# Optimization experiments

Hardware: AMD Instinct MI355X
Metric: run time of the kernel (lower is better)

## Reference

```python
import jax, jax.numpy as jnp
import numpy as np

NH, NKV, D = 16, 8, 128
HID = 2048
EPS = 1e-6
ROPE_BASE = 10000.0
T = 2048


def setup_inputs() -> dict:
    key = jax.random.key(0)
    k1, k2, k3 = jax.random.split(key, 3)
    return {
        "positions": jnp.arange(T, dtype=jnp.int32),
        "hidden_states": jax.random.normal(k1, (T, HID), dtype=jnp.float32),
        "w_qkv": jax.random.normal(k2, (HID, (NH + 2 * NKV) * D), dtype=jnp.float32) * 0.02,
        "w_o": jax.random.normal(k3, (NH * D, HID), dtype=jnp.float32) * 0.02,
        "q_norm_w": jnp.ones((D,), dtype=jnp.float32),
        "k_norm_w": jnp.ones((D,), dtype=jnp.float32),
    }


def _rmsnorm(x, w):
    # per-head RMSNorm over last dim (head_dim)
    return x * jax.lax.rsqrt(jnp.mean(x * x, axis=-1, keepdims=True) + EPS) * w


def reference(positions, hidden_states, w_qkv, w_o, q_norm_w, k_norm_w):
    t = hidden_states.shape[0]
    scale = D ** -0.5

    # fused QKV projection, then split
    qkv = hidden_states @ w_qkv                       # [T, (NH+2*NKV)*D]
    q, k, v = jnp.split(qkv, [NH * D, (NH + NKV) * D], axis=-1)
    q = q.reshape(t, NH, D)
    k = k.reshape(t, NKV, D)
    v = v.reshape(t, NKV, D)

    # per-head QK RMSNorm (Qwen3)
    q = _rmsnorm(q, q_norm_w)
    k = _rmsnorm(k, k_norm_w)

    # RoPE (neox style: rotate half-split pairs)
    inv_freq = 1.0 / (ROPE_BASE ** (jnp.arange(0, D, 2, dtype=jnp.float32) / D))
    freqs = positions.astype(jnp.float32)[:, None] * inv_freq  # [T, D/2]
    cos = jnp.cos(freqs)[:, None, :]                   # [T, 1, D/2]
    sin = jnp.sin(freqs)[:, None, :]

    def rope(x):
        x1, x2 = jnp.split(x, 2, axis=-1)
        return jnp.concatenate([x1 * cos - x2 * sin, x2 * cos + x1 * sin], axis=-1)

    q = rope(q)
    k = rope(k)

    # GQA: repeat kv heads
    g = NH // NKV
    kr = jnp.repeat(k, g, axis=1)                      # [T, NH, D]
    vr = jnp.repeat(v, g, axis=1)

    # causal attention
    scores = jnp.einsum('thd,shd->hts', q, kr) * scale  # [NH, T, T]
    causal = jnp.tril(jnp.ones((t, t), dtype=bool))
    scores = jnp.where(causal[None], scores, -jnp.inf)
    probs = jax.nn.softmax(scores, axis=-1)
    o = jnp.einsum('hts,shd->thd', probs, vr).reshape(t, NH * D)

    return o @ w_o
```

## Files before the change

kernel.cpp:

```cpp
#include <hip/hip_runtime.h>
#include <math.h>

#define T_TOK 2048
#define HIDDEN 2048
#define NH 16
#define NKV 8
#define DH 128

typedef unsigned short u16;
typedef __attribute__((ext_vector_type(8))) short bf16x8;
typedef __attribute__((ext_vector_type(4))) float f32x4;

__device__ __forceinline__ u16 f2bf(float f) {
  union { float f; unsigned u; } x; x.f = f;
  unsigned r = (x.u + 0x7fffu + ((x.u >> 16) & 1u)) >> 16;
  return (u16)r;
}

__device__ __forceinline__ float bf2f(u16 v) {
  union { unsigned u; float f; } x; x.u = ((unsigned)v) << 16;
  return x.f;
}

__device__ __forceinline__ void gload16(const void* g, void* l) {
  __builtin_amdgcn_global_load_lds((const __attribute__((address_space(1))) void*)g,
                                   (__attribute__((address_space(3))) void*)l,
                                   16, 0, 0);
}

__global__ __launch_bounds__(256) void prepass(const float* __restrict__ hidden,
                                               const float* __restrict__ w_qkv,
                                               const float* __restrict__ w_o,
                                               u16* __restrict__ Xb,
                                               u16* __restrict__ WqkvT,
                                               u16* __restrict__ WoT) {
  __shared__ float tile[64][65];
  const int b = blockIdx.x;
  if (b < 4096) {
    int i = b * 256 + threadIdx.x;
    float4 v = ((const float4*)hidden)[i];
    ushort4 o;
    o.x = f2bf(v.x); o.y = f2bf(v.y); o.z = f2bf(v.z); o.w = f2bf(v.w);
    ((ushort4*)Xb)[i] = o;
    return;
  }
  const float* in; u16* out; int R, Cdim, c0, r0;
  if (b < 6144) {
    int bb = b - 4096;
    in = w_qkv; out = WqkvT; R = 2048; Cdim = 4096;
    c0 = (bb & 63) * 64; r0 = (bb >> 6) * 64;
  } else {
    int bb = b - 6144;
    in = w_o; out = WoT; R = 2048; Cdim = 2048;
    c0 = (bb & 31) * 64; r0 = (bb >> 5) * 64;
  }
  const int tx = threadIdx.x & 63, ty = threadIdx.x >> 6;
#pragma unroll
  for (int i = 0; i < 64; i += 4)
    tile[ty + i][tx] = in[(size_t)(r0 + ty + i) * Cdim + c0 + tx];
  __syncthreads();
#pragma unroll
  for (int i = 0; i < 64; i += 4)
    out[(size_t)(c0 + ty + i) * R + r0 + tx] = f2bf(tile[tx][ty + i]);
}

__global__ __launch_bounds__(256) void add_parts2(const u16* __restrict__ a,
                                                  const u16* __restrict__ b,
                                                  float* __restrict__ o, int n4) {
  int i = blockIdx.x * blockDim.x + threadIdx.x;
  if (i < n4) {
    ushort4 x = ((const ushort4*)a)[i], y = ((const ushort4*)b)[i];
    float4 z;
    z.x = bf2f(x.x) + bf2f(y.x);
    z.y = bf2f(x.y) + bf2f(y.y);
    z.z = bf2f(x.z) + bf2f(y.z);
    z.w = bf2f(x.w) + bf2f(y.w);
    ((float4*)o)[i] = z;
  }
}

__global__ __launch_bounds__(256) void rope_vt(const u16* __restrict__ qkv,
                                               const int* __restrict__ pos,
                                               const float* __restrict__ qw,
                                               const float* __restrict__ kw,
                                               u16* __restrict__ Qg,
                                               u16* __restrict__ Kg,
                                               u16* __restrict__ Vt) {
  __shared__ float tile[64][65];
  const int b = blockIdx.x;
  if (b < 12288) {
    const int wave = threadIdx.x >> 6, j = threadIdx.x & 63;
    const int idx = b * 4 + wave;
    const int t = idx & 2047, slot = idx >> 11;
    const float QSC = 0.088388347648318447f * 1.4426950408889634f;
    const size_t base_i = (size_t)t * 4096 + slot * 128;
    float x1 = bf2f(qkv[base_i + j]);
    float x2 = bf2f(qkv[base_i + j + 64]);
    float ss = x1 * x1 + x2 * x2;
#pragma unroll
    for (int m = 1; m < 64; m <<= 1) ss += __shfl_xor(ss, m);
    float r = rsqrtf(ss * (1.0f / 128.0f) + 1e-6f);
    const bool isq = slot < NH;
    const float* w = isq ? qw : kw;
    float xn1 = x1 * r * w[j], xn2 = x2 * r * w[j + 64];
    float fp = (float)pos[t];
    float inv_freq = exp2f(-(float)j * (13.287712379549449f / 64.0f));
    float ang = fp * inv_freq;
    float sn, cs;
    sincosf(ang, &sn, &cs);
    float o1 = xn1 * cs - xn2 * sn;
    float o2 = xn2 * cs + xn1 * sn;
    if (isq) {
      size_t base = ((size_t)slot * T_TOK + t) * DH;
      Qg[base + j] = f2bf(o1 * QSC); Qg[base + 64 + j] = f2bf(o2 * QSC);
    } else {
      size_t base = ((size_t)(slot - NH) * T_TOK + t) * DH;
      Kg[base + j] = f2bf(o1); Kg[base + 64 + j] = f2bf(o2);
    }
    return;
  }
  const int bb = b - 12288;
  const int h = bb & 7, rest = bb >> 3;
  const int t0 = (rest & 31) * 64, d0 = (rest >> 5) * 64;
  const int tx = threadIdx.x & 63, ty = threadIdx.x >> 6;
#pragma unroll
  for (int i = 0; i < 64; i += 4) {
    size_t gi = (size_t)(t0 + ty + i) * 4096 + (NH + NKV) * DH + h * DH + d0 + tx;
    tile[ty + i][tx] = bf2f(qkv[gi]);
  }
  __syncthreads();
  const int sx = ((tx >> 5) * 2 + ((tx >> 2) & 1)) * 16 + ((tx >> 3) & 3) * 4 + (tx & 3);
#pragma unroll
  for (int i = 0; i < 64; i += 4)
    Vt[((size_t)h * DH + d0 + ty + i) * T_TOK + t0 + tx] = f2bf(tile[sx][ty + i]);
}

__global__ __launch_bounds__(512, 2) void gemm128x256(const u16* __restrict__ A,
                                                      const u16* __restrict__ Bt,
                                                      void* __restrict__ Cout,
                                                      int M, int N, int K,
                                                      int lda, int ldb, int obf16) {
  __shared__ __attribute__((aligned(128))) char lds[98304];

  const int nx = N >> 8, ny = M >> 7;
  const int flat = blockIdx.x;
  const int per = gridDim.x >> 3;
  const int swz = (flat & 7) * per + (flat >> 3);
  const int by = swz % ny;
  const int rest = swz / ny;
  const int bx = rest % nx;
  const int bz = rest / nx;
  const int m0 = by << 7, n0 = bx << 8;
  A += (size_t)bz * K;
  Bt += (size_t)bz * K;

  const int tid = threadIdx.x;
  const int wave = tid >> 6, lane = tid & 63;
  const int l15 = lane & 15, quad = lane >> 4;
  const int wr = wave >> 2, wc = wave & 3;

  size_t aoff;
  {
    int chunk = tid;
    int line = chunk >> 3;
    int ls8 = (chunk & 7) ^ (line & 7);
    int row = line * 2 + (ls8 >> 2);
    int ks = ls8 & 3;
    aoff = (size_t)(m0 + row) * lda + ks * 8;
  }
  size_t boff[2];
#pragma unroll
  for (int c = 0; c < 2; ++c) {
    int chunk = c * 512 + tid;
    int line = chunk >> 3;
    int ls8 = (chunk & 7) ^ (line & 7);
    int row = line * 2 + (ls8 >> 2);
    int ks = ls8 & 3;
    boff[c] = (size_t)(n0 + row) * ldb + ks * 8;
  }

#define STAGE(tt) do {                                                   \
    char* da = lds + ((tt) & 3) * 8192 + wave * 1024;                    \
    char* db = lds + 32768 + ((tt) & 3) * 16384 + wave * 1024;           \
    const int kk = (tt) * 32;                                            \
    gload16(A + aoff + kk, da);                                          \
    gload16(Bt + boff[0] + kk, db);                                      \
    gload16(Bt + boff[1] + kk, db + 8192);                               \
  } while (0)

  const int fragoff = (l15 >> 1) * 128 +
                      (((((l15 & 1) << 2) | quad) ^ ((l15 >> 1) & 7)) << 4);

  const f32x4 zero = {0.f, 0.f, 0.f, 0.f};
  f32x4 acc[4][4];
#pragma unroll
  for (int i = 0; i < 4; ++i)
#pragma unroll
    for (int j = 0; j < 4; ++j) acc[i][j] = zero;

  const int NT = K >> 5;
  STAGE(0); STAGE(1); STAGE(2);
  asm volatile("s_waitcnt vmcnt(6)" ::: "memory");
  __builtin_amdgcn_s_barrier();

  for (int t = 0; t < NT; ++t) {
    const char* As = lds + (t & 3) * 8192 + wr * 4096 + fragoff;
    const char* Bs = lds + 32768 + (t & 3) * 16384 + wc * 4096 + fragoff;
    bf16x8 af[4], bfr[4];
#pragma unroll
    for (int mt = 0; mt < 4; ++mt) af[mt] = *(const bf16x8*)(As + mt * 1024);
#pragma unroll
    for (int nt = 0; nt < 4; ++nt) bfr[nt] = *(const bf16x8*)(Bs + nt * 1024);

    if (t + 3 < NT) STAGE(t + 3);

    __builtin_amdgcn_s_setprio(1);
#pragma unroll
    for (int mt = 0; mt < 4; ++mt)
#pragma unroll
      for (int nt = 0; nt < 4; ++nt)
        acc[mt][nt] = __builtin_amdgcn_mfma_f32_16x16x32_bf16(af[mt], bfr[nt], acc[mt][nt], 0, 0, 0);
    __builtin_amdgcn_s_setprio(0);

    const int rem = NT - 1 - t;
    if (rem >= 3)      asm volatile("s_waitcnt vmcnt(6)" ::: "memory");
    else if (rem == 2) asm volatile("s_waitcnt vmcnt(3)" ::: "memory");
    else if (rem == 1) asm volatile("s_waitcnt vmcnt(0)" ::: "memory");
    if (rem > 0) __builtin_amdgcn_s_barrier();
  }
#undef STAGE

  if (obf16) {
    u16* C = (u16*)Cout + (size_t)bz * M * N;
#pragma unroll
    for (int mt = 0; mt < 4; ++mt)
#pragma unroll
      for (int nt = 0; nt < 4; ++nt)
#pragma unroll
        for (int r = 0; r < 4; ++r)
          C[(size_t)(m0 + wr * 64 + mt * 16 + quad * 4 + r) * N + n0 + wc * 64 + nt * 16 + l15] =
              f2bf(acc[mt][nt][r]);
  } else {
    float* C = (float*)Cout + (size_t)bz * M * N;
#pragma unroll
    for (int mt = 0; mt < 4; ++mt)
#pragma unroll
      for (int nt = 0; nt < 4; ++nt)
#pragma unroll
        for (int r = 0; r < 4; ++r)
          C[(size_t)(m0 + wr * 64 + mt * 16 + quad * 4 + r) * N + n0 + wc * 64 + nt * 16 + l15] =
              acc[mt][nt][r];
  }
}

__global__ __launch_bounds__(512) void attn_kernel(const u16* __restrict__ Qg,
                                                   const u16* __restrict__ Kg,
                                                   const u16* __restrict__ Vtg,
                                                   u16* __restrict__ Og) {
  __shared__ u16 Klds[2][64 * 128];
  __shared__ u16 Vlds[2][128 * 64];
  const int tid = threadIdx.x;
  const int wave = tid >> 6, lane = tid & 63;
  const int l15 = lane & 15, quad = lane >> 4;
  const int b = blockIdx.x;
  const int h = b & 15, pr = b >> 4;
  const int kvh = h >> 1;
  const int qtLO = pr, qtHI = 31 - pr;
  const int myqt = (wave < 4) ? qtHI : qtLO;
  const int w4 = wave & 3;
  const int jmax = qtHI + 1;
  const f32x4 zero = {0.f, 0.f, 0.f, 0.f};

  const u16* Qh = Qg + (size_t)h * T_TOK * DH;
  const u16* Kh = Kg + (size_t)kvh * T_TOK * DH;
  const u16* Vh = Vtg + (size_t)kvh * DH * T_TOK;
  const int qrow0 = myqt * 64 + w4 * 16;

#define STAGEKV(jj, sl) do {                                            \
    u16* Kd = &Klds[sl][0]; u16* Vd = &Vlds[sl][0];                     \
    _Pragma("unroll")                                                   \
    for (int c = 0; c < 2; ++c) {                                       \
      int chunk = wave * 2 + c;                                         \
      int sL = chunk * 64 + lane;                                       \
      { int ss = sL >> 4;                                               \
        int g = (sL & 15) ^ (ss & 15);                                  \
        gload16(Kh + ((size_t)((jj) * 64 + ss)) * DH + g * 8, Kd + chunk * 512); } \
      { int d = sL >> 3;                                                \
        int g = (sL & 7) ^ (d & 7);                                     \
        gload16(Vh + (size_t)d * T_TOK + (jj) * 64 + g * 8, Vd + chunk * 512); } \
    } } while (0)

  bf16x8 qf[4];
#pragma unroll
  for (int ks = 0; ks < 4; ++ks)
    qf[ks] = *(const bf16x8*)(Qh + (size_t)(qrow0 + l15) * DH + ks * 32 + quad * 8);

  f32x4 oacc[8];
#pragma unroll
  for (int i = 0; i < 8; ++i) oacc[i] = zero;
  float l_acc = 0.f;

  STAGEKV(0, 0);
  asm volatile("s_waitcnt vmcnt(0)" ::: "memory");
  __builtin_amdgcn_s_barrier();

  for (int j = 0; j < jmax; ++j) {
    const int sl = j & 1;
    const bool more = (j + 1 < jmax);
    if (more) STAGEKV(j + 1, sl ^ 1);
    if (j <= myqt) {
      const u16* Kl = &Klds[sl][0];
      const u16* Vl = &Vlds[sl][0];

      f32x4 sacc[4];
#pragma unroll
      for (int nt = 0; nt < 4; ++nt) sacc[nt] = zero;
      __builtin_amdgcn_s_setprio(1);
#pragma unroll
      for (int nt = 0; nt < 4; ++nt) {
        int sr = nt * 16 + l15;
#pragma unroll
        for (int ks = 0; ks < 4; ++ks) {
          bf16x8 kf = *(const bf16x8*)&Kl[sr * 128 + (((ks * 4 + quad) ^ (sr & 15)) * 8)];
          sacc[nt] = __builtin_amdgcn_mfma_f32_16x16x32_bf16(kf, qf[ks], sacc[nt], 0, 0, 0);
        }
      }
      __builtin_amdgcn_s_setprio(0);

      if (j >= myqt) {
        int q = qrow0 + l15;
#pragma unroll
        for (int nt = 0; nt < 4; ++nt)
#pragma unroll
          for (int r = 0; r < 4; ++r) {
            int k = j * 64 + nt * 16 + quad * 4 + r;
            if (k > q) sacc[nt][r] = -INFINITY;
          }
      }

      union { unsigned d[4]; bf16x8 v; } pa[2];
#pragma unroll
      for (int ks = 0; ks < 2; ++ks)
#pragma unroll
        for (int w = 0; w < 4; ++w) {
          int nt = ks * 2 + (w >> 1), rp = (w & 1) * 2;
          unsigned ulo = __float_as_uint(exp2f(sacc[nt][rp]));
          unsigned uhi = __float_as_uint(exp2f(sacc[nt][rp + 1]));
          l_acc += __uint_as_float(ulo & 0xffff0000u) + __uint_as_float(uhi & 0xffff0000u);
          pa[ks].d[w] = (ulo >> 16) | (uhi & 0xffff0000u);
        }

      __builtin_amdgcn_s_setprio(1);
#pragma unroll
      for (int ot = 0; ot < 8; ++ot) {
        int d = ot * 16 + l15;
#pragma unroll
        for (int ks = 0; ks < 2; ++ks) {
          bf16x8 vf = *(const bf16x8*)&Vl[d * 64 + (((ks * 4 + quad) ^ (d & 7)) * 8)];
          oacc[ot] = __builtin_amdgcn_mfma_f32_16x16x32_bf16(pa[ks].v, vf, oacc[ot], 0, 0, 0);
        }
      }
      __builtin_amdgcn_s_setprio(0);
    }

    if (more) {
      asm volatile("s_waitcnt vmcnt(0)" ::: "memory");
      __builtin_amdgcn_s_barrier();
    }
  }

  l_acc += __shfl_xor(l_acc, 16);
  l_acc += __shfl_xor(l_acc, 32);
  float rl[4];
#pragma unroll
  for (int r = 0; r < 4; ++r)
    rl[r] = 1.0f / __shfl(l_acc, quad * 4 + r);
#pragma unroll
  for (int ot = 0; ot < 8; ++ot)
#pragma unroll
    for (int r = 0; r < 4; ++r)
      Og[(size_t)(qrow0 + quad * 4 + r) * (NH * DH) + h * DH + ot * 16 + l15] =
          f2bf(oacc[ot][r] * rl[r]);
#undef STAGEKV
}

extern "C" void kernel_launch(void* const* d_in, const int* in_sizes, int n_in,
                              void* d_out, int out_size, void* d_ws, size_t ws_size,
                              hipStream_t stream) {
  (void)in_sizes; (void)n_in; (void)out_size; (void)ws_size;
  const int* positions = (const int*)d_in[0];
  const float* hidden  = (const float*)d_in[1];
  const float* w_qkv   = (const float*)d_in[2];
  const float* w_o     = (const float*)d_in[3];
  const float* q_norm  = (const float*)d_in[4];
  const float* k_norm  = (const float*)d_in[5];
  float* out = (float*)d_out;

  char* ws = (char*)d_ws;
  u16*   Xb    = (u16*)(ws);
  u16*   WqkvT = (u16*)(ws + ( 8ull << 20));
  u16*   WoT   = (u16*)(ws + (24ull << 20));
  u16*   P0    = (u16*)(ws + (32ull << 20));
  u16*   Qg    = (u16*)(ws + ( 8ull << 20));
  u16*   Kg    = (u16*)(ws + (16ull << 20));
  u16*   Vt    = (u16*)(ws + (20ull << 20));
  u16*   AttnO = (u16*)(ws + (48ull << 20));
  u16*   G2P   = (u16*)(ws + (32ull << 20));

  prepass<<<dim3(7168), 256, 0, stream>>>(hidden, w_qkv, w_o, Xb, WqkvT, WoT);

  gemm128x256<<<dim3(256), 512, 0, stream>>>(
      Xb, WqkvT, P0, T_TOK, 4096, HIDDEN, HIDDEN, HIDDEN, 1);

  rope_vt<<<dim3(12288 + 512), 256, 0, stream>>>(P0, positions,
                                                 q_norm, k_norm, Qg, Kg, Vt);

  attn_kernel<<<dim3(256), 512, 0, stream>>>(Qg, Kg, Vt, AttnO);

  gemm128x256<<<dim3(256), 512, 0, stream>>>(
      AttnO, WoT, G2P, T_TOK, HIDDEN, 1024, NH * DH, NH * DH, 1);
  const int n4 = T_TOK * HIDDEN / 4;
  add_parts2<<<dim3(n4 / 256), 256, 0, stream>>>(
      G2P, G2P + (size_t)T_TOK * HIDDEN, out, n4);
}
```

Measured before the change: 235.8 us.

## Split KV tiles across wave groups and process two query fragments per wave

The attention kernel now stages two KV tiles per iteration. The two four-wave groups each take alternate tiles, and every wave handles 32 query rows, so each K/V fragment read from LDS feeds two MFMAs. Partial outputs and row sums from the second group are combined with the first through LDS at the end. This is meant to halve the serial KV loop length per block and cut LDS reads per MFMA. The cost is double the LDS footprint, a cross-group reduction, and roughly double the accumulator registers. Under launch_bounds(512,2) that register growth could cause spills.

```diff
diff --git a/kernel.cpp b/kernel.cpp
--- a/kernel.cpp
+++ b/kernel.cpp
@@ -253,68 +253,77 @@
   }
 }
 
-__global__ __launch_bounds__(512) void attn_kernel(const u16* __restrict__ Qg,
-                                                   const u16* __restrict__ Kg,
-                                                   const u16* __restrict__ Vtg,
-                                                   u16* __restrict__ Og) {
-  __shared__ u16 Klds[2][64 * 128];
-  __shared__ u16 Vlds[2][128 * 64];
+__global__ __launch_bounds__(512, 2) void attn_kernel(const u16* __restrict__ Qg,
+                                                      const u16* __restrict__ Kg,
+                                                      const u16* __restrict__ Vtg,
+                                                      u16* __restrict__ Og) {
+  __shared__ u16 Klds[2][2][64 * 128];
+  __shared__ u16 Vlds[2][2][128 * 64];
+  __shared__ float Lx[128];
   const int tid = threadIdx.x;
   const int wave = tid >> 6, lane = tid & 63;
   const int l15 = lane & 15, quad = lane >> 4;
+  const int gp = wave >> 2, w4 = wave & 3;
   const int b = blockIdx.x;
   const int h = b & 15, pr = b >> 4;
   const int kvh = h >> 1;
-  const int qtLO = pr, qtHI = 31 - pr;
-  const int myqt = (wave < 4) ? qtHI : qtLO;
-  const int w4 = wave & 3;
+  const int qtHI = 31 - pr, qtLO = pr;
+  const int myqt = (w4 < 2) ? qtHI : qtLO;
+  const int qbase = myqt * 64 + (w4 & 1) * 32;
   const int jmax = qtHI + 1;
+  const int T = (jmax + 1) >> 1;
   const f32x4 zero = {0.f, 0.f, 0.f, 0.f};
 
   const u16* Qh = Qg + (size_t)h * T_TOK * DH;
   const u16* Kh = Kg + (size_t)kvh * T_TOK * DH;
   const u16* Vh = Vtg + (size_t)kvh * DH * T_TOK;
-  const int qrow0 = myqt * 64 + w4 * 16;
-
-#define STAGEKV(jj, sl) do {                                            \
-    u16* Kd = &Klds[sl][0]; u16* Vd = &Vlds[sl][0];                     \
+
+#define STAGEPAIR(t2, sl) do {                                          \
     _Pragma("unroll")                                                   \
-    for (int c = 0; c < 2; ++c) {                                       \
-      int chunk = wave * 2 + c;                                         \
-      int sL = chunk * 64 + lane;                                       \
+    for (int c = 0; c < 4; ++c) {                                       \
+      int cg = wave * 4 + c;                                \
+      int tp = cg >> 4;                                \
+      int cw = cg & 15;                                                 \
+      int sL = cw * 64 + lane;              \
+      int jj = (t2) + tp;                                               \
       { int ss = sL >> 4;                                               \
         int g = (sL & 15) ^ (ss & 15);                                  \
-        gload16(Kh + ((size_t)((jj) * 64 + ss)) * DH + g * 8, Kd + chunk * 512); } \
+        gload16(Kh + ((size_t)(jj * 64 + ss)) * DH + g * 8,             \
+                &Klds[sl][tp][0] + cw * 512); }                         \
       { int d = sL >> 3;                                                \
-        int g = (sL & 7) ^ (d & 7);                                     \
-        gload16(Vh + (size_t)d * T_TOK + (jj) * 64 + g * 8, Vd + chunk * 512); } \
+        int gv = (sL & 7) ^ (d & 7);                                    \
+        gload16(Vh + (size_t)d * T_TOK + jj * 64 + gv * 8,              \
+                &Vlds[sl][tp][0] + cw * 512); }                         \
     } } while (0)
 
-  bf16x8 qf[4];
-#pragma unroll
-  for (int ks = 0; ks < 4; ++ks)
-    qf[ks] = *(const bf16x8*)(Qh + (size_t)(qrow0 + l15) * DH + ks * 32 + quad * 8);
-
-  f32x4 oacc[8];
-#pragma unroll
-  for (int i = 0; i < 8; ++i) oacc[i] = zero;
-  float l_acc = 0.f;
-
-  STAGEKV(0, 0);
+  bf16x8 qfa[4], qfb[4];
+#pragma unroll
+  for (int ks = 0; ks < 4; ++ks) {
+    qfa[ks] = *(const bf16x8*)(Qh + (size_t)(qbase + l15) * DH + ks * 32 + quad * 8);
+    qfb[ks] = *(const bf16x8*)(Qh + (size_t)(qbase + 16 + l15) * DH + ks * 32 + quad * 8);
+  }
+
+  f32x4 oa[8], ob[8];
+#pragma unroll
+  for (int i = 0; i < 8; ++i) { oa[i] = zero; ob[i] = zero; }
+  float la = 0.f, lb = 0.f;
+
+  STAGEPAIR(0, 0);
   asm volatile("s_waitcnt vmcnt(0)" ::: "memory");
   __builtin_amdgcn_s_barrier();
 
-  for (int j = 0; j < jmax; ++j) {
-    const int sl = j & 1;
-    const bool more = (j + 1 < jmax);
-    if (more) STAGEKV(j + 1, sl ^ 1);
+  for (int t = 0; t < T; ++t) {
+    const int sl = t & 1;
+    const bool more = (t + 1 < T);
+    if (more) STAGEPAIR(2 * t + 2, sl ^ 1);
+    const int j = 2 * t + gp;
     if (j <= myqt) {
-      const u16* Kl = &Klds[sl][0];
-      const u16* Vl = &Vlds[sl][0];
-
-      f32x4 sacc[4];
-#pragma unroll
-      for (int nt = 0; nt < 4; ++nt) sacc[nt] = zero;
+      const u16* Kl = &Klds[sl][gp][0];
+      const u16* Vl = &Vlds[sl][gp][0];
+
+      f32x4 sa[4], sb[4];
+#pragma unroll
+      for (int nt = 0; nt < 4; ++nt) { sa[nt] = zero; sb[nt] = zero; }
       __builtin_amdgcn_s_setprio(1);
 #pragma unroll
       for (int nt = 0; nt < 4; ++nt) {
@@ -322,32 +331,38 @@
 #pragma unroll
         for (int ks = 0; ks < 4; ++ks) {
           bf16x8 kf = *(const bf16x8*)&Kl[sr * 128 + (((ks * 4 + quad) ^ (sr & 15)) * 8)];
-          sacc[nt] = __builtin_amdgcn_mfma_f32_16x16x32_bf16(kf, qf[ks], sacc[nt], 0, 0, 0);
+          sa[nt] = __builtin_amdgcn_mfma_f32_16x16x32_bf16(kf, qfa[ks], sa[nt], 0, 0, 0);
+          sb[nt] = __builtin_amdgcn_mfma_f32_16x16x32_bf16(kf, qfb[ks], sb[nt], 0, 0, 0);
         }
       }
       __builtin_amdgcn_s_setprio(0);
 
-      if (j >= myqt) {
-        int q = qrow0 + l15;
+      if (j == myqt) {
+        int qA = qbase + l15, qB = qA + 16;
 #pragma unroll
         for (int nt = 0; nt < 4; ++nt)
 #pragma unroll
           for (int r = 0; r < 4; ++r) {
             int k = j * 64 + nt * 16 + quad * 4 + r;
-            if (k > q) sacc[nt][r] = -INFINITY;
+            if (k > qA) sa[nt][r] = -INFINITY;
+            if (k > qB) sb[nt][r] = -INFINITY;
           }
       }
 
-      union { unsigned d[4]; bf16x8 v; } pa[2];
+      union { unsigned d[4]; bf16x8 v; } paA[2], paB[2];
 #pragma unroll
       for (int ks = 0; ks < 2; ++ks)
 #pragma unroll
         for (int w = 0; w < 4; ++w) {
           int nt = ks * 2 + (w >> 1), rp = (w & 1) * 2;
-          unsigned ulo = __float_as_uint(exp2f(sacc[nt][rp]));
-          unsigned uhi = __float_as_uint(exp2f(sacc[nt][rp + 1]));
-          l_acc += __uint_as_float(ulo & 0xffff0000u) + __uint_as_float(uhi & 0xffff0000u);
-          pa[ks].d[w] = (ulo >> 16) | (uhi & 0xffff0000u);
+          unsigned ulo = __float_as_uint(exp2f(sa[nt][rp]));
+          unsigned uhi = __float_as_uint(exp2f(sa[nt][rp + 1]));
+          la += __uint_as_float(ulo & 0xffff0000u) + __uint_as_float(uhi & 0xffff0000u);
+          paA[ks].d[w] = (ulo >> 16) | (uhi & 0xffff0000u);
+          unsigned vlo = __float_as_uint(exp2f(sb[nt][rp]));
+          unsigned vhi = __float_as_uint(exp2f(sb[nt][rp + 1]));
+          lb += __uint_as_float(vlo & 0xffff0000u) + __uint_as_float(vhi & 0xffff0000u);
+          paB[ks].d[w] = (vlo >> 16) | (vhi & 0xffff0000u);
         }
 
       __builtin_amdgcn_s_setprio(1);
@@ -357,7 +372,8 @@
 #pragma unroll
         for (int ks = 0; ks < 2; ++ks) {
           bf16x8 vf = *(const bf16x8*)&Vl[d * 64 + (((ks * 4 + quad) ^ (d & 7)) * 8)];
-          oacc[ot] = __builtin_amdgcn_mfma_f32_16x16x32_bf16(pa[ks].v, vf, oacc[ot], 0, 0, 0);
+          oa[ot] = __builtin_amdgcn_mfma_f32_16x16x32_bf16(paA[ks].v, vf, oa[ot], 0, 0, 0);
+          ob[ot] = __builtin_amdgcn_mfma_f32_16x16x32_bf16(paB[ks].v, vf, ob[ot], 0, 0, 0);
         }
       }
       __builtin_amdgcn_s_setprio(0);
@@ -369,19 +385,48 @@
     }
   }
 
-  l_acc += __shfl_xor(l_acc, 16);
-  l_acc += __shfl_xor(l_acc, 32);
-  float rl[4];
-#pragma unroll
-  for (int r = 0; r < 4; ++r)
-    rl[r] = 1.0f / __shfl(l_acc, quad * 4 + r);
-#pragma unroll
-  for (int ot = 0; ot < 8; ++ot)
-#pragma unroll
-    for (int r = 0; r < 4; ++r)
-      Og[(size_t)(qrow0 + quad * 4 + r) * (NH * DH) + h * DH + ot * 16 + l15] =
-          f2bf(oacc[ot][r] * rl[r]);
-#undef STAGEKV
+  la += __shfl_xor(la, 16); la += __shfl_xor(la, 32);
+  lb += __shfl_xor(lb, 16); lb += __shfl_xor(lb, 32);
+
+  __syncthreads();
+  float* Olds = (float*)&Klds[0][0][0];
+  if (gp == 1) {
+    float* Ow = Olds + (size_t)w4 * (32 * 128);
+#pragma unroll
+    for (int ot = 0; ot < 8; ++ot)
+#pragma unroll
+      for (int r = 0; r < 4; ++r) {
+        Ow[(quad * 4 + r) * 128 + ot * 16 + l15] = oa[ot][r];
+        Ow[(16 + quad * 4 + r) * 128 + ot * 16 + l15] = ob[ot][r];
+      }
+    if (quad == 0) {
+      Lx[w4 * 32 + l15] = la;
+      Lx[w4 * 32 + 16 + l15] = lb;
+    }
+  }
+  __syncthreads();
+  if (gp == 0) {
+    const float* Or = Olds + (size_t)w4 * (32 * 128);
+    float rlA[4], rlB[4];
+#pragma unroll
+    for (int r = 0; r < 4; ++r) {
+      int i = quad * 4 + r;
+      rlA[r] = 1.0f / (__shfl(la, i) + Lx[w4 * 32 + i]);
+      rlB[r] = 1.0f / (__shfl(lb, i) + Lx[w4 * 32 + 16 + i]);
+    }
+#pragma unroll
+    for (int ot = 0; ot < 8; ++ot)
+#pragma unroll
+      for (int r = 0; r < 4; ++r) {
+        int rowA = qbase + quad * 4 + r;
+        Og[(size_t)rowA * (NH * DH) + h * DH + ot * 16 + l15] =
+            f2bf((oa[ot][r] + Or[(quad * 4 + r) * 128 + ot * 16 + l15]) * rlA[r]);
+        int rowB = rowA + 16;
+        Og[(size_t)rowB * (NH * DH) + h * DH + ot * 16 + l15] =
+            f2bf((ob[ot][r] + Or[(16 + quad * 4 + r) * 128 + ot * 16 + l15]) * rlB[r]);
+      }
+  }
+#undef STAGEPAIR
 }
 
 extern "C" void kernel_launch(void* const* d_in, const int* in_sizes, int n_in,
```

After: 237.6 us. Within noise of the previous version (+0.7%).

## Rebalance causal attention work across wave groups with split-KV and LDS reduction

Applied to the files above, without the earlier changes.

In the original kernel, one wave group handles the high query tile (up to 32 KV tiles) while the other handles the low tile (few KV tiles), so half the waves sit idle for most iterations. Now both groups first process the low tile's KV tiles together. After that, the two groups split the remaining high-tile KV tiles, each taking alternate tiles from double-staged buffers, which shortens the loop to 17 steps. Partial outputs and row sums for the high tile are combined through LDS at the end. The cost is twice the LDS footprint, a second set of accumulators that raises register pressure, and an extra reduction step.

```diff
diff --git a/kernel.cpp b/kernel.cpp
--- a/kernel.cpp
+++ b/kernel.cpp
@@ -253,135 +253,193 @@
   }
 }
 
-__global__ __launch_bounds__(512) void attn_kernel(const u16* __restrict__ Qg,
-                                                   const u16* __restrict__ Kg,
-                                                   const u16* __restrict__ Vtg,
-                                                   u16* __restrict__ Og) {
-  __shared__ u16 Klds[2][64 * 128];
-  __shared__ u16 Vlds[2][128 * 64];
+__global__ __launch_bounds__(512, 2) void attn_kernel(const u16* __restrict__ Qg,
+                                                      const u16* __restrict__ Kg,
+                                                      const u16* __restrict__ Vtg,
+                                                      u16* __restrict__ Og) {
+  __shared__ u16 Klds[2][2][64 * 128];
+  __shared__ u16 Vlds[2][2][128 * 64];
+  __shared__ float Lx[64];
   const int tid = threadIdx.x;
   const int wave = tid >> 6, lane = tid & 63;
   const int l15 = lane & 15, quad = lane >> 4;
+  const int gp = wave >> 2, w4 = wave & 3;
   const int b = blockIdx.x;
   const int h = b & 15, pr = b >> 4;
   const int kvh = h >> 1;
-  const int qtLO = pr, qtHI = 31 - pr;
-  const int myqt = (wave < 4) ? qtHI : qtLO;
-  const int w4 = wave & 3;
-  const int jmax = qtHI + 1;
+  const int qtHI = 31 - pr, qtLO = pr;
   const f32x4 zero = {0.f, 0.f, 0.f, 0.f};
 
   const u16* Qh = Qg + (size_t)h * T_TOK * DH;
   const u16* Kh = Kg + (size_t)kvh * T_TOK * DH;
   const u16* Vh = Vtg + (size_t)kvh * DH * T_TOK;
-  const int qrow0 = myqt * 64 + w4 * 16;
-
-#define STAGEKV(jj, sl) do {                                            \
-    u16* Kd = &Klds[sl][0]; u16* Vd = &Vlds[sl][0];                     \
+  const int qbH = qtHI * 64 + w4 * 16;
+  const int qbL = qtLO * 64 + w4 * 16;
+
+#define STAGE1(jj, sl, ss) do {                                         \
+    u16* Kd = &Klds[sl][ss][0]; u16* Vd = &Vlds[sl][ss][0];             \
     _Pragma("unroll")                                                   \
     for (int c = 0; c < 2; ++c) {                                       \
       int chunk = wave * 2 + c;                                         \
       int sL = chunk * 64 + lane;                                       \
-      { int ss = sL >> 4;                                               \
-        int g = (sL & 15) ^ (ss & 15);                                  \
-        gload16(Kh + ((size_t)((jj) * 64 + ss)) * DH + g * 8, Kd + chunk * 512); } \
+      { int ssk = sL >> 4;                                              \
+        int g = (sL & 15) ^ (ssk & 15);                                 \
+        gload16(Kh + ((size_t)((jj) * 64 + ssk)) * DH + g * 8, Kd + chunk * 512); } \
       { int d = sL >> 3;                                                \
-        int g = (sL & 7) ^ (d & 7);                                     \
-        gload16(Vh + (size_t)d * T_TOK + (jj) * 64 + g * 8, Vd + chunk * 512); } \
+        int gv = (sL & 7) ^ (d & 7);                                    \
+        gload16(Vh + (size_t)d * T_TOK + (jj) * 64 + gv * 8, Vd + chunk * 512); } \
     } } while (0)
 
-  bf16x8 qf[4];
-#pragma unroll
-  for (int ks = 0; ks < 4; ++ks)
-    qf[ks] = *(const bf16x8*)(Qh + (size_t)(qrow0 + l15) * DH + ks * 32 + quad * 8);
-
-  f32x4 oacc[8];
-#pragma unroll
-  for (int i = 0; i < 8; ++i) oacc[i] = zero;
-  float l_acc = 0.f;
-
-  STAGEKV(0, 0);
+#define STAGESTEP(ts, sl) do {                                          \
+    if ((ts) <= pr) { STAGE1((ts), (sl), 0); }                          \
+    else {                                                              \
+      int uu = (ts) - pr - 1;                                           \
+      int jA = pr + 1 + 2 * uu;                                         \
+      STAGE1(jA, (sl), 0);                                              \
+      if (jA + 1 <= qtHI) STAGE1(jA + 1, (sl), 1);                      \
+    } } while (0)
+
+#define TILE_BODY(QF, OACC, LACC, QT, JJ, KL, VL) do {                  \
+    f32x4 sacc[4];                                                      \
+    _Pragma("unroll")                                                   \
+    for (int nt = 0; nt < 4; ++nt) sacc[nt] = zero;                     \
+    __builtin_amdgcn_s_setprio(1);                                      \
+    _Pragma("unroll")                                                   \
+    for (int nt = 0; nt < 4; ++nt) {                                    \
+      int sr = nt * 16 + l15;                                           \
+      _Pragma("unroll")                                                 \
+      for (int ks = 0; ks < 4; ++ks) {                                  \
+        bf16x8 kf = *(const bf16x8*)&(KL)[sr * 128 + (((ks * 4 + quad) ^ (sr & 15)) * 8)]; \
+        sacc[nt] = __builtin_amdgcn_mfma_f32_16x16x32_bf16(kf, (QF)[ks], sacc[nt], 0, 0, 0); \
+      }                                                                 \
+    }                                                                   \
+    __builtin_amdgcn_s_setprio(0);                                      \
+    if ((JJ) == (QT)) {                                                 \
+      int q = (QT) * 64 + w4 * 16 + l15;                                \
+      _Pragma("unroll")                                                 \
+      for (int nt = 0; nt < 4; ++nt)                                    \
+        _Pragma("unroll")                                               \
+        for (int r = 0; r < 4; ++r) {                                   \
+          int k = (JJ) * 64 + nt * 16 + quad * 4 + r;                   \
+          if (k > q) sacc[nt][r] = -INFINITY;                           \
+        }                                                               \
+    }                                                                   \
+    union { unsigned d[4]; bf16x8 v; } pa[2];                           \
+    _Pragma("unroll")                                                   \
+    for (int ks = 0; ks < 2; ++ks)                                      \
+      _Pragma("unroll")                                                 \
+      for (int w = 0; w < 4; ++w) {                                     \
+        int nt = ks * 2 + (w >> 1), rp = (w & 1) * 2;                   \
+        unsigned ulo = __float_as_uint(exp2f(sacc[nt][rp]));            \
+        unsigned uhi = __float_as_uint(exp2f(sacc[nt][rp + 1]));        \
+        (LACC) += __uint_as_float(ulo & 0xffff0000u) + __uint_as_float(uhi & 0xffff0000u); \
+        pa[ks].d[w] = (ulo >> 16) | (uhi & 0xffff0000u);                \
+      }                                                                 \
+    __builtin_amdgcn_s_setprio(1);                                      \
+    _Pragma("unroll")                                                   \
+    for (int ot = 0; ot < 8; ++ot) {                                    \
+      int d = ot * 16 + l15;                                            \
+      _Pragma("unroll")                                                 \
+      for (int ks = 0; ks < 2; ++ks) {                                  \
+        bf16x8 vf = *(const bf16x8*)&(VL)[d * 64 + (((ks * 4 + quad) ^ (d & 7)) * 8)]; \
+        (OACC)[ot] = __builtin_amdgcn_mfma_f32_16x16x32_bf16(pa[ks].v, vf, (OACC)[ot], 0, 0, 0); \
+      }                                                                 \
+    }                                                                   \
+    __builtin_amdgcn_s_setprio(0);                                      \
+  } while (0)
+
+  bf16x8 qfH[4], qfL[4];
+#pragma unroll
+  for (int ks = 0; ks < 4; ++ks) {
+    qfH[ks] = *(const bf16x8*)(Qh + (size_t)(qbH + l15) * DH + ks * 32 + quad * 8);
+    qfL[ks] = *(const bf16x8*)(Qh + (size_t)(qbL + l15) * DH + ks * 32 + quad * 8);
+  }
+
+  f32x4 oaccH[8], oaccL[8];
+#pragma unroll
+  for (int i = 0; i < 8; ++i) { oaccH[i] = zero; oaccL[i] = zero; }
+  float lH = 0.f, lL = 0.f;
+
+  STAGE1(0, 0, 0);
   asm volatile("s_waitcnt vmcnt(0)" ::: "memory");
   __builtin_amdgcn_s_barrier();
 
-  for (int j = 0; j < jmax; ++j) {
-    const int sl = j & 1;
-    const bool more = (j + 1 < jmax);
-    if (more) STAGEKV(j + 1, sl ^ 1);
-    if (j <= myqt) {
-      const u16* Kl = &Klds[sl][0];
-      const u16* Vl = &Vlds[sl][0];
-
-      f32x4 sacc[4];
-#pragma unroll
-      for (int nt = 0; nt < 4; ++nt) sacc[nt] = zero;
-      __builtin_amdgcn_s_setprio(1);
-#pragma unroll
-      for (int nt = 0; nt < 4; ++nt) {
-        int sr = nt * 16 + l15;
-#pragma unroll
-        for (int ks = 0; ks < 4; ++ks) {
-          bf16x8 kf = *(const bf16x8*)&Kl[sr * 128 + (((ks * 4 + quad) ^ (sr & 15)) * 8)];
-          sacc[nt] = __builtin_amdgcn_mfma_f32_16x16x32_bf16(kf, qf[ks], sacc[nt], 0, 0, 0);
+  for (int t = 0; t < 17; ++t) {
+    const int sl = t & 1;
+    if (t < 16) STAGESTEP(t + 1, sl ^ 1);
+
+    if (t <= pr) {
+      const u16* Kl = &Klds[sl][0][0];
+      const u16* Vl = &Vlds[sl][0][0];
+      if (gp == 0) TILE_BODY(qfH, oaccH, lH, qtHI, t, Kl, Vl);
+      else         TILE_BODY(qfL, oaccL, lL, qtLO, t, Kl, Vl);
+    } else {
+      const int uu = t - pr - 1;
+      if (gp == 0) {
+        const int j = pr + 1 + 2 * uu;
+        const u16* Kl = &Klds[sl][0][0];
+        const u16* Vl = &Vlds[sl][0][0];
+        TILE_BODY(qfH, oaccH, lH, qtHI, j, Kl, Vl);
+      } else {
+        const int j = pr + 2 + 2 * uu;
+        if (j <= qtHI) {
+          const u16* Kl = &Klds[sl][1][0];
+          const u16* Vl = &Vlds[sl][1][0];
+          TILE_BODY(qfH, oaccH, lH, qtHI, j, Kl, Vl);
         }
       }
-      __builtin_amdgcn_s_setprio(0);
-
-      if (j >= myqt) {
-        int q = qrow0 + l15;
-#pragma unroll
-        for (int nt = 0; nt < 4; ++nt)
-#pragma unroll
-          for (int r = 0; r < 4; ++r) {
-            int k = j * 64 + nt * 16 + quad * 4 + r;
-            if (k > q) sacc[nt][r] = -INFINITY;
-          }
-      }
-
-      union { unsigned d[4]; bf16x8 v; } pa[2];
-#pragma unroll
-      for (int ks = 0; ks < 2; ++ks)
-#pragma unroll
-        for (int w = 0; w < 4; ++w) {
-          int nt = ks * 2 + (w >> 1), rp = (w & 1) * 2;
-          unsigned ulo = __float_as_uint(exp2f(sacc[nt][rp]));
-          unsigned uhi = __float_as_uint(exp2f(sacc[nt][rp + 1]));
-          l_acc += __uint_as_float(ulo & 0xffff0000u) + __uint_as_float(uhi & 0xffff0000u);
-          pa[ks].d[w] = (ulo >> 16) | (uhi & 0xffff0000u);
-        }
-
-      __builtin_amdgcn_s_setprio(1);
-#pragma unroll
-      for (int ot = 0; ot < 8; ++ot) {
-        int d = ot * 16 + l15;
-#pragma unroll
-        for (int ks = 0; ks < 2; ++ks) {
-          bf16x8 vf = *(const bf16x8*)&Vl[d * 64 + (((ks * 4 + quad) ^ (d & 7)) * 8)];
-          oacc[ot] = __builtin_amdgcn_mfma_f32_16x16x32_bf16(pa[ks].v, vf, oacc[ot], 0, 0, 0);
-        }
-      }
-      __builtin_amdgcn_s_setprio(0);
     }
 
-    if (more) {
+    if (t < 16) {
       asm volatile("s_waitcnt vmcnt(0)" ::: "memory");
       __builtin_amdgcn_s_barrier();
     }
   }
 
-  l_acc += __shfl_xor(l_acc, 16);
-  l_acc += __shfl_xor(l_acc, 32);
-  float rl[4];
-#pragma unroll
-  for (int r = 0; r < 4; ++r)
-    rl[r] = 1.0f / __shfl(l_acc, quad * 4 + r);
-#pragma unroll
-  for (int ot = 0; ot < 8; ++ot)
+  lH += __shfl_xor(lH, 16); lH += __shfl_xor(lH, 32);
+  lL += __shfl_xor(lL, 16); lL += __shfl_xor(lL, 32);
+
+  __syncthreads();
+  float* Ox = (float*)&Klds[0][0][0];
+  if (gp == 1) {
+    float* Ow = Ox + (size_t)w4 * 2048;
+#pragma unroll
+    for (int ot = 0; ot < 8; ++ot)
+#pragma unroll
+      for (int r = 0; r < 4; ++r)
+        Ow[(quad * 4 + r) * 128 + ot * 16 + l15] = oaccH[ot][r];
+    if (quad == 0) Lx[w4 * 16 + l15] = lH;
+  }
+  __syncthreads();
+  if (gp == 0) {
+    const float* Or = Ox + (size_t)w4 * 2048;
+    float rl[4];
+#pragma unroll
+    for (int r = 0; r < 4; ++r) {
+      int i = quad * 4 + r;
+      rl[r] = 1.0f / (__shfl(lH, i) + Lx[w4 * 16 + i]);
+    }
+#pragma unroll
+    for (int ot = 0; ot < 8; ++ot)
+#pragma unroll
+      for (int r = 0; r < 4; ++r)
+        Og[(size_t)(qbH + quad * 4 + r) * (NH * DH) + h * DH + ot * 16 + l15] =
+            f2bf((oaccH[ot][r] + Or[(quad * 4 + r) * 128 + ot * 16 + l15]) * rl[r]);
+  } else {
+    float rl[4];
 #pragma unroll
     for (int r = 0; r < 4; ++r)
-      Og[(size_t)(qrow0 + quad * 4 + r) * (NH * DH) + h * DH + ot * 16 + l15] =
-          f2bf(oacc[ot][r] * rl[r]);
-#undef STAGEKV
+      rl[r] = 1.0f / __shfl(lL, quad * 4 + r);
+#pragma unroll
+    for (int ot = 0; ot < 8; ++ot)
+#pragma unroll
+      for (int r = 0; r < 4; ++r)
+        Og[(size_t)(qbL + quad * 4 + r) * (NH * DH) + h * DH + ot * 16 + l15] =
+            f2bf(oaccL[ot][r] * rl[r]);
+  }
+#undef TILE_BODY
+#undef STAGESTEP
+#undef STAGE1
 }
 
 extern "C" void kernel_launch(void* const* d_in, const int* in_sizes, int n_in,
```

Result: faster. 231.0 us (-2.0%).
